# Performance work log

Hardware: AMD Instinct MI355X
Metric: run time of the kernel (lower is better)

## Reference

```python
import jax, jax.numpy as jnp
import numpy as np

N_ATOMS = 32768
DEG = 16            # directed neighbors per atom
N_RBF = 6
CUTOFF = 5.0
ENV_P = 6


def _build_graph():
    # circular-offset neighbor structure so every (j,i) / (k,j) pair in
    # angle_list exists exactly once in nbr_list (required by m_idx_of_angles)
    half = DEG // 2
    offs = np.concatenate([np.arange(1, half + 1), N_ATOMS - np.arange(1, half + 1)])  # [DEG]
    j = np.arange(N_ATOMS)
    nbr_dst = (j[:, None] + offs[None, :]) % N_ATOMS                    # [N, DEG]
    nbr_list = np.stack([np.repeat(j, DEG), nbr_dst.reshape(-1)], 1)    # [E, 2]
    o1, o2 = np.meshgrid(offs, offs, indexing='ij')
    keep = o1 != o2
    o1, o2 = o1[keep], o2[keep]                                         # [DEG*(DEG-1)]
    i = (j[:, None] + o1[None, :]) % N_ATOMS
    k = (j[:, None] + o2[None, :]) % N_ATOMS
    jc = np.broadcast_to(j[:, None], i.shape)
    angle_list = np.stack([i.reshape(-1), jc.reshape(-1), k.reshape(-1)], 1)  # [T, 3]
    return nbr_list.astype(np.int64), angle_list.astype(np.int64)


def setup_inputs() -> dict:
    key = jax.random.key(0)
    nbr, ang = _build_graph()
    xyz = jax.random.normal(key, (N_ATOMS, 3), dtype=jnp.float32) * 3.0
    return {"xyz": xyz, "nbr_list": jnp.asarray(nbr), "angle_list": jnp.asarray(ang)}


def _match_edge(nbr_list, src, dst):
    # efficient, mathematically identical replacement for the O(T*E)
    # broadcast-mask + nonzero() in m_idx_of_angles (each edge is unique)
    keys = nbr_list[:, 0] * N_ATOMS + nbr_list[:, 1]
    order = jnp.argsort(keys)
    pos = jnp.searchsorted(keys[order], src * N_ATOMS + dst)
    return order[pos]


def _envelope(x):
    p = ENV_P
    a = -(p + 1) * (p + 2) / 2.0
    b = float(p * (p + 2))
    c = -p * (p + 1) / 2.0
    return 1.0 / x + a * x ** (p - 1) + b * x ** p + c * x ** (p + 1)


def reference(xyz, nbr_list, angle_list):
    # --- edge distances ---
    diff = xyz[nbr_list[:, 0]] - xyz[nbr_list[:, 1]]          # [E, 3]
    d = jnp.linalg.norm(diff, axis=-1)                        # [E]
    # --- triplet angles (compute_angle) ---
    r_ji = xyz[angle_list[:, 0]] - xyz[angle_list[:, 1]]      # [T, 3]
    r_jk = xyz[angle_list[:, 2]] - xyz[angle_list[:, 1]]      # [T, 3]
    dot = jnp.sum(r_ji * r_jk, axis=-1)
    crs = jnp.linalg.norm(jnp.cross(r_ji, r_jk), axis=-1)
    alpha = jnp.arctan2(crs, dot)                             # [T]
    # --- radial basis with polynomial envelope ---
    n = jnp.arange(1, N_RBF + 1, dtype=xyz.dtype)
    dc = (d / CUTOFF)[:, None]                                # [E, 1]
    e_rbf = _envelope(dc) * jnp.sin(n * jnp.pi * dc)          # [E, N_RBF]
    # --- triplet->edge index matching (m_idx_of_angles) ---
    ji_idx = _match_edge(nbr_list, angle_list[:, 1], angle_list[:, 0])  # [T]
    kj_idx = _match_edge(nbr_list, angle_list[:, 2], angle_list[:, 1])  # [T]
    # --- gather-compute-scatter stage (interaction-block aggregation) ---
    trip = alpha[:, None] * e_rbf[kj_idx]                     # [T, N_RBF]
    out = jax.ops.segment_sum(trip, ji_idx, num_segments=nbr_list.shape[0])  # [E, N_RBF]
    return out
```

## Files before the change

kernel.cpp:

```cpp
#include <hip/hip_runtime.h>
#include <math.h>


constexpr int N_ATOMS = 32768;
constexpr int DEG = 16;
constexpr int N_RBF = 6;
constexpr int APB = 16;
constexpr float CUTOFF = 5.0f;

__global__ __launch_bounds__(256) void dimenet_fused(const float* __restrict__ xyz,
                                                     float* __restrict__ out) {
    const int tid = threadIdx.x;
    const int a   = tid >> 4;
    const int m   = tid & 15;
    const int j   = blockIdx.x * APB + a;

    __shared__ float4 s_rel[APB][DEG];
    __shared__ float4 s_rbf[APB][DEG][2];

    const int off = (m < 8) ? (m + 1) : (7 - m);
    const int nbr = (j + off + N_ATOMS) & (N_ATOMS - 1);

    const float jx = xyz[3 * j + 0], jy = xyz[3 * j + 1], jz = xyz[3 * j + 2];
    const float rx = xyz[3 * nbr + 0] - jx;
    const float ry = xyz[3 * nbr + 1] - jy;
    const float rz = xyz[3 * nbr + 2] - jz;
    const float d  = __builtin_amdgcn_sqrtf(rx * rx + ry * ry + rz * rz);
    s_rel[a][m] = make_float4(rx, ry, rz, d);

    const float x  = d * (1.0f / CUTOFF);
    const float x2 = x * x, x5 = x2 * x2 * x;
    const float env = __builtin_amdgcn_rcpf(x) + x5 * (-28.0f + x * (48.0f - 21.0f * x));

    float s1, c1;
    sincosf((float)M_PI * x, &s1, &c1);
    float sn = s1, cn = c1;
    float r0 = env * s1, r1, r2, r3, r4, r5;
    {
        float t;
        t = sn * c1 + cn * s1; cn = cn * c1 - sn * s1; sn = t; r1 = env * sn;
        t = sn * c1 + cn * s1; cn = cn * c1 - sn * s1; sn = t; r2 = env * sn;
        t = sn * c1 + cn * s1; cn = cn * c1 - sn * s1; sn = t; r3 = env * sn;
        t = sn * c1 + cn * s1; cn = cn * c1 - sn * s1; sn = t; r4 = env * sn;
        t = sn * c1 + cn * s1; cn = cn * c1 - sn * s1; sn = t; r5 = env * sn;
    }
    s_rbf[a][m][0] = make_float4(r0, r1, r2, r3);
    s_rbf[a][m][1] = make_float4(r4, r5, 0.f, 0.f);

    __syncthreads();

    const float C0 =  2.0f * 0.99997726f;
    const float C1 = -2.0f * 0.33262347f;
    const float C2 =  2.0f * 0.19354346f;
    const float C3 = -2.0f * 0.11643287f;
    const float C4 =  2.0f * 0.05265332f;
    const float C5 = -2.0f * 0.01172120f;
    const float PI_F = 3.14159265358979f;

    float acc0 = 0.f, acc1 = 0.f, acc2 = 0.f, acc3 = 0.f, acc4 = 0.f, acc5 = 0.f;

#pragma unroll
    for (int t = 1; t < DEG; ++t) {
        const int m2 = (m + t) & 15;
        const float4 rr = s_rel[a][m2];
        const float dot = rx * rr.x + ry * rr.y + rz * rr.z;
        const float u   = d * rr.w;
        const float num = u - dot;
        const float den = u + dot;
        float mn = fminf(num, den);
        float mx = fmaxf(num, den);
        mn = fmaxf(mn, 0.0f);
        mx = fmaxf(mx, 1e-30f);
        const float z  = __builtin_amdgcn_sqrtf(mn * __builtin_amdgcn_rcpf(mx));
        const float zs = z * z;
        float p = fmaf(zs, C5, C4);
        p = fmaf(zs, p, C3);
        p = fmaf(zs, p, C2);
        p = fmaf(zs, p, C1);
        p = fmaf(zs, p, C0);
        const float at2   = z * p;
        const float alpha = (num <= den) ? at2 : (PI_F - at2);

        const float4 b0 = s_rbf[a][m2][0];
        const float4 b1 = s_rbf[a][m2][1];
        acc0 = fmaf(alpha, b0.x, acc0);
        acc1 = fmaf(alpha, b0.y, acc1);
        acc2 = fmaf(alpha, b0.z, acc2);
        acc3 = fmaf(alpha, b0.w, acc3);
        acc4 = fmaf(alpha, b1.x, acc4);
        acc5 = fmaf(alpha, b1.y, acc5);
    }

    float2* o = (float2*)(out + (size_t)(j * DEG + m) * N_RBF);
    o[0] = make_float2(acc0, acc1);
    o[1] = make_float2(acc2, acc3);
    o[2] = make_float2(acc4, acc5);
}

extern "C" void kernel_launch(void* const* d_in, const int* in_sizes, int n_in,
                              void* d_out, int out_size, void* d_ws, size_t ws_size,
                              hipStream_t stream) {
    const float* xyz = (const float*)d_in[0];
    float* out = (float*)d_out;
    dim3 grid(N_ATOMS / APB);
    dim3 block(256);
    hipLaunchKernelGGL(dimenet_fused, grid, block, 0, stream, xyz, out);
}
```

Baseline: 132.2 us.

## Exploit angle symmetry to halve triplet angle evaluations via shared memory

Each neighbor pair's angle is symmetric, so each thread now computes angles only for offsets 1..8. The results for offsets 1..7 go into a padded shared array, and the other seven angles are read back from the partner thread after a barrier. The libm sincosf call is also replaced with the hardware sin/cos intrinsics on a range-reduced revolution argument. This trades about half of the atan2 arithmetic for extra LDS traffic and a second barrier, and the hardware trig may be slightly less accurate.

```diff
diff --git a/kernel.cpp b/kernel.cpp
--- a/kernel.cpp
+++ b/kernel.cpp
@@ -17,6 +17,7 @@
 
     __shared__ float4 s_rel[APB][DEG];
     __shared__ float4 s_rbf[APB][DEG][2];
+    __shared__ float  s_alpha[APB][7][17];
 
     const int off = (m < 8) ? (m + 1) : (7 - m);
     const int nbr = (j + off + N_ATOMS) & (N_ATOMS - 1);
@@ -32,8 +33,10 @@
     const float x2 = x * x, x5 = x2 * x2 * x;
     const float env = __builtin_amdgcn_rcpf(x) + x5 * (-28.0f + x * (48.0f - 21.0f * x));
 
-    float s1, c1;
-    sincosf((float)M_PI * x, &s1, &c1);
+    const float xr  = x * 0.5f;
+    const float rev = xr - floorf(xr);
+    const float s1  = __builtin_amdgcn_sinf(rev);
+    const float c1  = __builtin_amdgcn_cosf(rev);
     float sn = s1, cn = c1;
     float r0 = env * s1, r1, r2, r3, r4, r5;
     {
@@ -60,19 +63,17 @@
     float acc0 = 0.f, acc1 = 0.f, acc2 = 0.f, acc3 = 0.f, acc4 = 0.f, acc5 = 0.f;
 
 #pragma unroll
-    for (int t = 1; t < DEG; ++t) {
+    for (int t = 1; t <= 8; ++t) {
         const int m2 = (m + t) & 15;
         const float4 rr = s_rel[a][m2];
         const float dot = rx * rr.x + ry * rr.y + rz * rr.z;
         const float u   = d * rr.w;
-        const float num = u - dot;
-        const float den = u + dot;
-        float mn = fminf(num, den);
-        float mx = fmaxf(num, den);
-        mn = fmaxf(mn, 0.0f);
-        mx = fmaxf(mx, 1e-30f);
-        const float z  = __builtin_amdgcn_sqrtf(mn * __builtin_amdgcn_rcpf(mx));
-        const float zs = z * z;
+        const float num = fmaxf(u - dot, 0.0f);
+        const float den = fmaxf(u + dot, 0.0f);
+        const float mn  = fminf(num, den);
+        const float mx  = fmaxf(fmaxf(num, den), 1e-30f);
+        const float z   = __builtin_amdgcn_sqrtf(mn * __builtin_amdgcn_rcpf(mx));
+        const float zs  = z * z;
         float p = fmaf(zs, C5, C4);
         p = fmaf(zs, p, C3);
         p = fmaf(zs, p, C2);
@@ -81,6 +82,24 @@
         const float at2   = z * p;
         const float alpha = (num <= den) ? at2 : (PI_F - at2);
 
+        if (t < 8) s_alpha[a][t - 1][m] = alpha;
+
+        const float4 b0 = s_rbf[a][m2][0];
+        const float4 b1 = s_rbf[a][m2][1];
+        acc0 = fmaf(alpha, b0.x, acc0);
+        acc1 = fmaf(alpha, b0.y, acc1);
+        acc2 = fmaf(alpha, b0.z, acc2);
+        acc3 = fmaf(alpha, b0.w, acc3);
+        acc4 = fmaf(alpha, b1.x, acc4);
+        acc5 = fmaf(alpha, b1.y, acc5);
+    }
+
+    __syncthreads();
+
+#pragma unroll
+    for (int t = 9; t <= 15; ++t) {
+        const int m2 = (m + t) & 15;
+        const float alpha = s_alpha[a][15 - t][m2];
         const float4 b0 = s_rbf[a][m2][0];
         const float4 b1 = s_rbf[a][m2][1];
         acc0 = fmaf(alpha, b0.x, acc0);
```

Result: no change. 130.1 us (-1.6%).
